# Optimization experiments

Measured on AMD Instinct MI355X. Metric: run time of the kernel, lower is better.

## Reference

```python
import jax, jax.numpy as jnp
import numpy as np

BASIS_PRIMES = (2, 3, 5, 7, 11, 13, 17, 19, 23, 29)


def _build_resonance(max_seq):
    # p-adic valuations v_p(n) for n = 1..max_seq, each basis prime (vectorized LUT build)
    n = np.arange(1, max_seq + 1, dtype=np.int64)
    vals = np.zeros((max_seq, len(BASIS_PRIMES)), dtype=np.float32)
    for j, p in enumerate(BASIS_PRIMES):
        m = n.copy()
        while True:
            div = (m % p) == 0
            if not div.any():
                break
            vals[div, j] += 1.0
            m = np.where(div, m // p, m)
    # resonance(a,b) = sum_i min(v_{p_i}(a), v_{p_i}(b))  -> [T, T]
    res = np.zeros((max_seq, max_seq), dtype=np.float32)
    for j in range(len(BASIS_PRIMES)):
        vj = vals[:, j]
        res += np.minimum(vj[:, None], vj[None, :])
    causal = np.tril(np.ones((max_seq, max_seq), dtype=bool))
    allowed = ((res > 0) | np.eye(max_seq, dtype=bool)) & causal
    bias = (np.log1p(res) * allowed).astype(np.float32)
    return bias, allowed


def setup_inputs() -> dict:
    B, T, d_model, head_size, max_seq = 8, 2048, 1024, 128, 2048
    key = jax.random.key(0)
    kx, kq, kk, kv = jax.random.split(key, 4)
    bound = 1.0 / np.sqrt(d_model)  # torch Linear default init range
    x = jax.random.normal(kx, (B, T, d_model), dtype=jnp.float32)
    Wq = jax.random.uniform(kq, (head_size, d_model), jnp.float32, -bound, bound)
    Wk = jax.random.uniform(kk, (head_size, d_model), jnp.float32, -bound, bound)
    Wv = jax.random.uniform(kv, (head_size, d_model), jnp.float32, -bound, bound)
    bias, allowed = _build_resonance(max_seq)
    return {
        "x": x, "Wq": Wq, "Wk": Wk, "Wv": Wv,
        "resonance_bias": jnp.asarray(bias),
        "allowed": jnp.asarray(allowed),
    }


def reference(x, Wq, Wk, Wv, resonance_bias, allowed):
    B, T, C = x.shape
    q = jnp.einsum('btc,hc->bth', x, Wq)
    k = jnp.einsum('btc,hc->bth', x, Wk)
    v = jnp.einsum('btc,hc->bth', x, Wv)
    # NOTE: original scales by C**-0.5 where C = d_model (input channels)
    wei = jnp.einsum('bth,bsh->bts', q, k) * (C ** -0.5)
    wei = wei + resonance_bias[:T, :T]
    neg = jnp.finfo(wei.dtype).min
    wei = jnp.where(allowed[:T, :T], wei, neg)
    wei = jax.nn.softmax(wei, axis=-1)  # dropout is identity in eval mode
    return jnp.einsum('bts,bsh->bth', wei, v)
```

## Files before the change

### kernel.cpp

```cpp
#include <hip/hip_runtime.h>
#include <hip/hip_bf16.h>
#include <stdint.h>

typedef float f32x4  __attribute__((ext_vector_type(4)));
typedef short s16x8  __attribute__((ext_vector_type(8)));
typedef short s16x4  __attribute__((ext_vector_type(4)));
typedef unsigned short u16x8 __attribute__((ext_vector_type(8)));

#define MFMA16(A,B,C) __builtin_amdgcn_mfma_f32_16x16x32_bf16((A),(B),(C),0,0,0)

__device__ __forceinline__ short f2bf(float f) {
    uint32_t u = __float_as_uint(f);
    u += 0x7FFFu + ((u >> 16) & 1u);
    return (short)(u >> 16);
}
__device__ __forceinline__ float bf2f(unsigned short u) {
    return __uint_as_float(((uint32_t)u) << 16);
}
__device__ __forceinline__ int cum_jobs(int qt) {
  int h = qt >> 1;
  return (qt & 1) ? (h + 1) * (h + 1) : h * (h + 1);
}

#define OFF_PB   0u
#define OFF_WPK  8388608u
#define OFF_PQ   9175040u
#define OFF_PK   13369344u
#define OFF_PV   17563648u
#define OFF_XPK  21757952u
#define OFF_PML  21757952u
#define OFF_PO   22863872u
#define WS_SPLIT 60096512u

__global__ __launch_bounds__(256) void pack_w_kernel(
    const float* __restrict__ wq, const float* __restrict__ wk,
    const float* __restrict__ wv, short* __restrict__ Wpk) {
  const int tid = threadIdx.x, wid = tid >> 6, lane = tid & 63;
  const int g = lane >> 4, c4 = lane & 15;
  const int idx = blockIdx.x * 4 + wid;
  const int im = idx >> 8, rest = idx & 255;
  const int ntl = rest >> 5, k32 = rest & 31;
  const float* w = (im == 0) ? wq : (im == 1) ? wk : wv;
  const float* p = w + (size_t)(ntl * 16 + c4) * 1024 + k32 * 32 + 4 * g;
  f32x4 lo = *(const f32x4*)p;
  f32x4 hi = *(const f32x4*)(p + 16);
  s16x8 o = { f2bf(lo[0]), f2bf(lo[1]), f2bf(lo[2]), f2bf(lo[3]),
              f2bf(hi[0]), f2bf(hi[1]), f2bf(hi[2]), f2bf(hi[3]) };
  *(s16x8*)(Wpk + (size_t)idx * 512 + lane * 8) = o;
}

__global__ __launch_bounds__(256) void pack_x_kernel(
    const float* __restrict__ x, short* __restrict__ xpk) {
  const int tid = threadIdx.x, wid = tid >> 6, lane = tid & 63;
  const int g = lane >> 4, c4 = lane & 15;
  const int idx = blockIdx.x * 4 + wid;
  const int m16 = idx >> 5, k32 = idx & 31;
  const float* p = x + (size_t)(m16 * 16 + c4) * 1024 + k32 * 32 + 4 * g;
  f32x4 lo = *(const f32x4*)p;
  f32x4 hi = *(const f32x4*)(p + 16);
  s16x8 o = { f2bf(lo[0]), f2bf(lo[1]), f2bf(lo[2]), f2bf(lo[3]),
              f2bf(hi[0]), f2bf(hi[1]), f2bf(hi[2]), f2bf(hi[3]) };
  *(s16x8*)(xpk + (size_t)idx * 512 + lane * 8) = o;
}

__global__ __launch_bounds__(256) void pack_bias_kernel(
    const float* __restrict__ bias, short* __restrict__ pb) {
  const int tid = threadIdx.x, wid = tid >> 6, lane = tid & 63;
  const int g = lane >> 4, c4 = lane & 15;
  const int idx = blockIdx.x * 4 + wid;
  const int t16 = idx >> 6, s32 = idx & 63;
  const int t = t16 * 16 + c4;
  const int sb = s32 * 32 + 4 * g;
  const float* p = bias + (size_t)t * 2048 + sb;
  f32x4 lo = *(const f32x4*)p;
  f32x4 hi = *(const f32x4*)(p + 16);
  s16x8 o;
  #pragma unroll
  for (int i = 0; i < 4; ++i) {
    int s0 = sb + i, s1 = sb + 16 + i;
    bool ok0 = (s0 <= t) && (s0 == t || lo[i] > 0.f);
    bool ok1 = (s1 <= t) && (s1 == t || hi[i] > 0.f);
    o[i]     = f2bf(ok0 ? lo[i] : -1e30f);
    o[4 + i] = f2bf(ok1 ? hi[i] : -1e30f);
  }
  *(s16x8*)(pb + (size_t)idx * 512 + lane * 8) = o;
}

__global__ __launch_bounds__(256, 3) void qkv_gemm6_kernel(
    const short* __restrict__ xpk, const short* __restrict__ Wpk,
    short* __restrict__ pq, short* __restrict__ pk, short* __restrict__ pv) {
  const int tid = threadIdx.x, wid = tid >> 6, lane = tid & 63;
  const int L8 = lane * 8;
  const int w = blockIdx.x * 4 + wid;
  const int im = w >> 9;
  const int t2 = w & 511;
  const int b = t2 >> 6;
  const short* xa = xpk + (size_t)(t2 * 64) * 512 + L8;
  const short* xb = xa + (size_t)32 * 512;
  const short* wp = Wpk + (size_t)(im * 256) * 512 + L8;

  f32x4 acc0[8], acc1[8];
  #pragma unroll
  for (int i = 0; i < 8; ++i) {
    acc0[i] = (f32x4){0.f, 0.f, 0.f, 0.f};
    acc1[i] = (f32x4){0.f, 0.f, 0.f, 0.f};
  }

  s16x8 xA0, xA1, wA[8], xB0, xB1, wB[8];
#define G6_LDX(d0, d1, kk) { d0 = *(const s16x8*)(xa + (size_t)(kk) * 512); \
                             d1 = *(const s16x8*)(xb + (size_t)(kk) * 512); }
#define G6_LDW(dw, kk) { _Pragma("unroll") \
    for (int nt = 0; nt < 8; ++nt) \
      dw[nt] = *(const s16x8*)(wp + (size_t)(nt * 32 + (kk)) * 512); }

  if (im < 2) {
    G6_LDX(xA0, xA1, 0); G6_LDW(wA, 0);
    for (int k = 0; k < 32; k += 2) {
      G6_LDX(xB0, xB1, k + 1); G6_LDW(wB, k + 1);
      #pragma unroll
      for (int nt = 0; nt < 8; ++nt) {
        acc0[nt] = MFMA16(wA[nt], xA0, acc0[nt]);
        acc1[nt] = MFMA16(wA[nt], xA1, acc1[nt]);
      }
      if (k + 2 < 32) { G6_LDX(xA0, xA1, k + 2); G6_LDW(wA, k + 2); }
      #pragma unroll
      for (int nt = 0; nt < 8; ++nt) {
        acc0[nt] = MFMA16(wB[nt], xB0, acc0[nt]);
        acc1[nt] = MFMA16(wB[nt], xB1, acc1[nt]);
      }
    }
    short* __restrict__ o = im ? pk : pq;
    const int loc0 = (t2 & 63) * 2;
    #pragma unroll
    for (int f = 0; f < 4; ++f) {
      s16x8 fr0 = { f2bf(acc0[2*f][0]),   f2bf(acc0[2*f][1]),
                    f2bf(acc0[2*f][2]),   f2bf(acc0[2*f][3]),
                    f2bf(acc0[2*f+1][0]), f2bf(acc0[2*f+1][1]),
                    f2bf(acc0[2*f+1][2]), f2bf(acc0[2*f+1][3]) };
      *(s16x8*)(o + (size_t)(b * 512 + loc0 * 4 + f) * 512 + L8) = fr0;
      s16x8 fr1 = { f2bf(acc1[2*f][0]),   f2bf(acc1[2*f][1]),
                    f2bf(acc1[2*f][2]),   f2bf(acc1[2*f][3]),
                    f2bf(acc1[2*f+1][0]), f2bf(acc1[2*f+1][1]),
                    f2bf(acc1[2*f+1][2]), f2bf(acc1[2*f+1][3]) };
      *(s16x8*)(o + (size_t)(b * 512 + (loc0 + 1) * 4 + f) * 512 + L8) = fr1;
    }
  } else {
    G6_LDX(xA0, xA1, 0); G6_LDW(wA, 0);
    for (int k = 0; k < 32; k += 2) {
      G6_LDX(xB0, xB1, k + 1); G6_LDW(wB, k + 1);
      #pragma unroll
      for (int nt = 0; nt < 8; ++nt) {
        acc0[nt] = MFMA16(xA0, wA[nt], acc0[nt]);
        acc1[nt] = MFMA16(xA1, wA[nt], acc1[nt]);
      }
      if (k + 2 < 32) { G6_LDX(xA0, xA1, k + 2); G6_LDW(wA, k + 2); }
      #pragma unroll
      for (int nt = 0; nt < 8; ++nt) {
        acc0[nt] = MFMA16(xB0, wB[nt], acc0[nt]);
        acc1[nt] = MFMA16(xB1, wB[nt], acc1[nt]);
      }
    }
    const int s32l = t2 & 63;
    #pragma unroll
    for (int nt = 0; nt < 8; ++nt) {
      s16x8 fr = { f2bf(acc0[nt][0]), f2bf(acc0[nt][1]),
                   f2bf(acc0[nt][2]), f2bf(acc0[nt][3]),
                   f2bf(acc1[nt][0]), f2bf(acc1[nt][1]),
                   f2bf(acc1[nt][2]), f2bf(acc1[nt][3]) };
      *(s16x8*)(pv + (size_t)(b * 512 + s32l * 8 + nt) * 512 + L8) = fr;
    }
  }
#undef G6_LDX
#undef G6_LDW
}

template<bool SPLIT>
__global__ __launch_bounds__(128) void attn_kernel(
    const short* __restrict__ pq, const short* __restrict__ pk,
    const short* __restrict__ pv, const short* __restrict__ pb,
    float* __restrict__ out, float* __restrict__ part_ml,
    short* __restrict__ part_o) {
  int qt, c;
  if (SPLIT) {
    const int i = blockIdx.x;
    int h = (int)sqrtf((float)i);
    while (h * h > i) --h;
    while ((h + 1) * (h + 1) <= i) ++h;
    if (i < h * (h + 1)) { qt = 2 * h - 1; c = i - h * h; }
    else                 { qt = 2 * h;     c = i - h * (h + 1); }
  } else {
    qt = blockIdx.x; c = 0;
  }
  const int n = (qt >> 1) + 1;
  const int tid = threadIdx.x;
  const int wid = tid >> 6, lane = tid & 63;
  const int g = lane >> 4, c4 = lane & 15;
  const int b = blockIdx.y;
  const int q16a = qt * 4 + wid * 2;
  const int L8 = lane * 8;

  s16x8 qfa[4], qfb[4];
  #pragma unroll
  for (int f = 0; f < 4; ++f) {
    qfa[f] = *(const s16x8*)(pq + (size_t)(b * 512 + q16a * 4 + f) * 512 + L8);
    qfb[f] = *(const s16x8*)(pq + (size_t)(b * 512 + (q16a + 1) * 4 + f) * 512 + L8);
  }

  float m0 = -1e30f, l0 = 0.f, m1 = -1e30f, l1 = 0.f;
  f32x4 acc0[8], acc1[8];
  #pragma unroll
  for (int i = 0; i < 8; ++i) {
    acc0[i] = (f32x4){0.f, 0.f, 0.f, 0.f};
    acc1[i] = (f32x4){0.f, 0.f, 0.f, 0.f};
  }

  const int q_hi_w = qt * 64 + wid * 32 + 32;
  const int s_begin = SPLIT ? c * 128 : 0;
  const int s_stop  = min(SPLIT ? s_begin + 128 : (1 << 30), q_hi_w);

  for (int s0 = s_begin; s0 < s_stop; s0 += 32) {
    const int s16i = s0 >> 4, s32 = s0 >> 5;
    const short* kbase = pk + (size_t)(b * 512 + s16i * 4) * 512 + L8;
    const short* vbase = pv + (size_t)(b * 512 + s32 * 8) * 512 + L8;
    s16x8 kf0[4], kf1[4];
    #pragma unroll
    for (int f = 0; f < 4; ++f) {
      kf0[f] = *(const s16x8*)(kbase + (size_t)f * 512);
      kf1[f] = *(const s16x8*)(kbase + (size_t)(4 + f) * 512);
    }
    u16x8 bva = *(const u16x8*)(pb + (size_t)(q16a * 64 + s32) * 512 + L8);
    u16x8 bvb = *(const u16x8*)(pb + (size_t)((q16a + 1) * 64 + s32) * 512 + L8);
    f32x4 s0a = (f32x4){0.f,0.f,0.f,0.f}, s1a = (f32x4){0.f,0.f,0.f,0.f};
    f32x4 s0b = (f32x4){0.f,0.f,0.f,0.f}, s1b = (f32x4){0.f,0.f,0.f,0.f};
    __builtin_amdgcn_s_setprio(1);
    #pragma unroll
    for (int f = 0; f < 4; ++f) {
      s0a = MFMA16(kf0[f], qfa[f], s0a);
      s1a = MFMA16(kf1[f], qfa[f], s1a);
      s0b = MFMA16(kf0[f], qfb[f], s0b);
      s1b = MFMA16(kf1[f], qfb[f], s1b);
    }
    __builtin_amdgcn_s_setprio(0);
    float va[8], vb[8];
    #pragma unroll
    for (int st = 0; st < 2; ++st)
      #pragma unroll
      for (int r = 0; r < 4; ++r) {
        va[st * 4 + r] = (st ? s1a[r] : s0a[r]) * 0.03125f + bf2f(bva[st * 4 + r]);
        vb[st * 4 + r] = (st ? s1b[r] : s0b[r]) * 0.03125f + bf2f(bvb[st * 4 + r]);
      }
    float mva = va[0], mvb = vb[0];
    #pragma unroll
    for (int i = 1; i < 8; ++i) { mva = fmaxf(mva, va[i]); mvb = fmaxf(mvb, vb[i]); }
    mva = fmaxf(mva, __shfl_xor(mva, 16)); mva = fmaxf(mva, __shfl_xor(mva, 32));
    mvb = fmaxf(mvb, __shfl_xor(mvb, 16)); mvb = fmaxf(mvb, __shfl_xor(mvb, 32));
    if (!__all((mva <= m0 + 8.f) && (mvb <= m1 + 8.f))) {
      float mn0 = fmaxf(m0, mva), mn1 = fmaxf(m1, mvb);
      float a0 = __expf(m0 - mn0), a1 = __expf(m1 - mn1);
      l0 *= a0; l1 *= a1; m0 = mn0; m1 = mn1;
      float ar0[4], ar1[4];
      #pragma unroll
      for (int r = 0; r < 4; ++r) {
        ar0[r] = __shfl(a0, (lane & 48) | (4 * g + r));
        ar1[r] = __shfl(a1, (lane & 48) | (4 * g + r));
      }
      #pragma unroll
      for (int nt = 0; nt < 8; ++nt)
        #pragma unroll
        for (int r = 0; r < 4; ++r) {
          acc0[nt][r] *= ar0[r];
          acc1[nt][r] *= ar1[r];
        }
    }
    float pa8[8], pb8[8], psa = 0.f, psb = 0.f;
    #pragma unroll
    for (int i = 0; i < 8; ++i) {
      pa8[i] = (va[i] > -1e29f) ? __expf(va[i] - m0) : 0.f;  psa += pa8[i];
      pb8[i] = (vb[i] > -1e29f) ? __expf(vb[i] - m1) : 0.f;  psb += pb8[i];
    }
    psa += __shfl_xor(psa, 16); psa += __shfl_xor(psa, 32); l0 += psa;
    psb += __shfl_xor(psb, 16); psb += __shfl_xor(psb, 32); l1 += psb;
    s16x8 paf = { f2bf(pa8[0]), f2bf(pa8[1]), f2bf(pa8[2]), f2bf(pa8[3]),
                  f2bf(pa8[4]), f2bf(pa8[5]), f2bf(pa8[6]), f2bf(pa8[7]) };
    s16x8 pbf = { f2bf(pb8[0]), f2bf(pb8[1]), f2bf(pb8[2]), f2bf(pb8[3]),
                  f2bf(pb8[4]), f2bf(pb8[5]), f2bf(pb8[6]), f2bf(pb8[7]) };
    __builtin_amdgcn_s_setprio(1);
    #pragma unroll
    for (int nt = 0; nt < 8; ++nt) {
      s16x8 vf = *(const s16x8*)(vbase + (size_t)nt * 512);
      acc0[nt] = MFMA16(paf, vf, acc0[nt]);
      acc1[nt] = MFMA16(pbf, vf, acc1[nt]);
    }
    __builtin_amdgcn_s_setprio(0);
  }

  if (!SPLIT || n == 1) {
    float li0 = 1.f / l0, li1 = 1.f / l1;
    float lr0[4], lr1[4];
    #pragma unroll
    for (int r = 0; r < 4; ++r) {
      lr0[r] = __shfl(li0, (lane & 48) | (4 * g + r));
      lr1[r] = __shfl(li1, (lane & 48) | (4 * g + r));
    }
    const int row0 = qt * 64 + wid * 32;
    #pragma unroll
    for (int nt = 0; nt < 8; ++nt)
      #pragma unroll
      for (int r = 0; r < 4; ++r) {
        out[(size_t)(b * 2048 + row0 + 4 * g + r) * 128 + 16 * nt + c4] =
            acc0[nt][r] * lr0[r];
        out[(size_t)(b * 2048 + row0 + 16 + 4 * g + r) * 128 + 16 * nt + c4] =
            acc1[nt][r] * lr1[r];
      }
  } else {
    const int slot = b * 270 + cum_jobs(qt) - 2 + c;
    short* po = part_o + (size_t)slot * 8192 + (size_t)(wid * 8) * 512 + L8;
    #pragma unroll
    for (int nt = 0; nt < 8; ++nt) {
      s16x8 fr = { f2bf(acc0[nt][0]), f2bf(acc0[nt][1]),
                   f2bf(acc0[nt][2]), f2bf(acc0[nt][3]),
                   f2bf(acc1[nt][0]), f2bf(acc1[nt][1]),
                   f2bf(acc1[nt][2]), f2bf(acc1[nt][3]) };
      *(s16x8*)(po + (size_t)nt * 512) = fr;
    }
    if (lane < 16) {
      part_ml[slot * 128 + wid * 32 + c4]           = m0;
      part_ml[slot * 128 + wid * 32 + 16 + c4]      = m1;
      part_ml[slot * 128 + 64 + wid * 32 + c4]      = l0;
      part_ml[slot * 128 + 64 + wid * 32 + 16 + c4] = l1;
    }
  }
}

__global__ __launch_bounds__(256) void combine_kernel(
    const float* __restrict__ part_ml, const unsigned short* __restrict__ part_o,
    float* __restrict__ out) {
  const int qt = 2 + blockIdx.x;
  const int b = blockIdx.y;
  const int n = (qt >> 1) + 1;
  const int slot0 = b * 270 + cum_jobs(qt) - 2;
  const int tid = threadIdx.x;

  __shared__ float scl[16][64];
  if (tid < 64) {
    const int r = tid;
    float M = -1e30f;
    for (int cc = 0; cc < n; ++cc)
      M = fmaxf(M, part_ml[(size_t)(slot0 + cc) * 128 + r]);
    float L = 0.f;
    for (int cc = 0; cc < n; ++cc)
      L += part_ml[(size_t)(slot0 + cc) * 128 + 64 + r] *
           __expf(part_ml[(size_t)(slot0 + cc) * 128 + r] - M);
    float inv = 1.f / L;
    for (int cc = 0; cc < n; ++cc)
      scl[cc][r] = __expf(part_ml[(size_t)(slot0 + cc) * 128 + r] - M) * inv;
  }
  __syncthreads();
  const int fgr = tid >> 6, lane = tid & 63;
  const int g = lane >> 4, c4 = lane & 15;
  for (int ff = fgr; ff < 16; ff += 4) {
    const int rbase = (ff >> 3) * 32 + 4 * g;
    const int col = (ff & 7) * 16 + c4;
    float o[8] = {0.f,0.f,0.f,0.f,0.f,0.f,0.f,0.f};
    for (int cc = 0; cc < n; ++cc) {
      u16x8 v = *(const u16x8*)(part_o +
          (size_t)(slot0 + cc) * 8192 + (size_t)ff * 512 + lane * 8);
      #pragma unroll
      for (int j = 0; j < 8; ++j)
        o[j] += bf2f(v[j]) * scl[cc][rbase + (j >> 2) * 16 + (j & 3)];
    }
    #pragma unroll
    for (int j = 0; j < 8; ++j) {
      const int row = rbase + (j >> 2) * 16 + (j & 3);
      out[(size_t)(b * 2048 + qt * 64 + row) * 128 + col] = o[j];
    }
  }
}

extern "C" void kernel_launch(void* const* d_in, const int* in_sizes, int n_in,
                              void* d_out, int out_size, void* d_ws, size_t ws_size,
                              hipStream_t stream) {
  const float* x    = (const float*)d_in[0];
  const float* wq   = (const float*)d_in[1];
  const float* wk   = (const float*)d_in[2];
  const float* wv   = (const float*)d_in[3];
  const float* bias = (const float*)d_in[4];

  char* ws = (char*)d_ws;
  short* pb      = (short*)(ws + OFF_PB);
  short* Wpk     = (short*)(ws + OFF_WPK);
  short* pq      = (short*)(ws + OFF_PQ);
  short* pk      = (short*)(ws + OFF_PK);
  short* pv      = (short*)(ws + OFF_PV);
  short* xpk     = (short*)(ws + OFF_XPK);
  float* part_ml = (float*)(ws + OFF_PML);
  short* part_o  = (short*)(ws + OFF_PO);
  float* outp    = (float*)d_out;

  pack_w_kernel<<<192, 256, 0, stream>>>(wq, wk, wv, Wpk);
  pack_x_kernel<<<8192, 256, 0, stream>>>(x, xpk);
  qkv_gemm6_kernel<<<384, 256, 0, stream>>>(xpk, Wpk, pq, pk, pv);
  pack_bias_kernel<<<2048, 256, 0, stream>>>(bias, pb);

  if (ws_size >= WS_SPLIT) {
    attn_kernel<true><<<dim3(272, 8), 128, 0, stream>>>(
        pq, pk, pv, pb, outp, part_ml, part_o);
    combine_kernel<<<dim3(30, 8), 256, 0, stream>>>(
        part_ml, (const unsigned short*)part_o, outp);
  } else {
    attn_kernel<false><<<dim3(32, 8), 128, 0, stream>>>(
        pq, pk, pv, pb, outp, part_ml, part_o);
  }
}
```

Measured before the change: 104.2 us.

## Fuse x bf16 conversion into QKV GEMM and merge weight/bias packing

The QKV GEMM now reads fp32 x directly and converts it to bf16 in registers, so the separate pack_x pass and its bf16 intermediate buffer go away. The weight and bias packing kernels are merged into a single launch, cutting launch count from four pre-attention kernels to two. In exchange, the GEMM loads twice the bytes for x, has to do the conversion inside its loop, and uses more registers (launch bounds occupancy hint lowered from 3 to 2). Each x row is read by three projection waves, so the raw fp32 x traffic is repeated.

Result: slower. 109.2 us (+4.8%).

```diff
diff --git a/kernel.cpp b/kernel.cpp
--- a/kernel.cpp
+++ b/kernel.cpp
@@ -27,76 +27,60 @@
 #define OFF_PQ   9175040u
 #define OFF_PK   13369344u
 #define OFF_PV   17563648u
-#define OFF_XPK  21757952u
 #define OFF_PML  21757952u
 #define OFF_PO   22863872u
 #define WS_SPLIT 60096512u
 
-__global__ __launch_bounds__(256) void pack_w_kernel(
+__global__ __launch_bounds__(256) void pack_misc_kernel(
     const float* __restrict__ wq, const float* __restrict__ wk,
-    const float* __restrict__ wv, short* __restrict__ Wpk) {
+    const float* __restrict__ wv, const float* __restrict__ bias,
+    short* __restrict__ Wpk, short* __restrict__ pb) {
   const int tid = threadIdx.x, wid = tid >> 6, lane = tid & 63;
   const int g = lane >> 4, c4 = lane & 15;
-  const int idx = blockIdx.x * 4 + wid;
-  const int im = idx >> 8, rest = idx & 255;
-  const int ntl = rest >> 5, k32 = rest & 31;
-  const float* w = (im == 0) ? wq : (im == 1) ? wk : wv;
-  const float* p = w + (size_t)(ntl * 16 + c4) * 1024 + k32 * 32 + 4 * g;
-  f32x4 lo = *(const f32x4*)p;
-  f32x4 hi = *(const f32x4*)(p + 16);
-  s16x8 o = { f2bf(lo[0]), f2bf(lo[1]), f2bf(lo[2]), f2bf(lo[3]),
-              f2bf(hi[0]), f2bf(hi[1]), f2bf(hi[2]), f2bf(hi[3]) };
-  *(s16x8*)(Wpk + (size_t)idx * 512 + lane * 8) = o;
-}
-
-__global__ __launch_bounds__(256) void pack_x_kernel(
-    const float* __restrict__ x, short* __restrict__ xpk) {
+  if (blockIdx.x < 192) {
+    const int idx = blockIdx.x * 4 + wid;
+    const int im = idx >> 8, rest = idx & 255;
+    const int ntl = rest >> 5, k32 = rest & 31;
+    const float* w = (im == 0) ? wq : (im == 1) ? wk : wv;
+    const float* p = w + (size_t)(ntl * 16 + c4) * 1024 + k32 * 32 + 4 * g;
+    f32x4 lo = *(const f32x4*)p;
+    f32x4 hi = *(const f32x4*)(p + 16);
+    s16x8 o = { f2bf(lo[0]), f2bf(lo[1]), f2bf(lo[2]), f2bf(lo[3]),
+                f2bf(hi[0]), f2bf(hi[1]), f2bf(hi[2]), f2bf(hi[3]) };
+    *(s16x8*)(Wpk + (size_t)idx * 512 + lane * 8) = o;
+  } else {
+    const int idx = (blockIdx.x - 192) * 4 + wid;
+    const int t16 = idx >> 6, s32 = idx & 63;
+    const int t = t16 * 16 + c4;
+    const int sb = s32 * 32 + 4 * g;
+    const float* p = bias + (size_t)t * 2048 + sb;
+    f32x4 lo = *(const f32x4*)p;
+    f32x4 hi = *(const f32x4*)(p + 16);
+    s16x8 o;
+    #pragma unroll
+    for (int i = 0; i < 4; ++i) {
+      int s0 = sb + i, s1 = sb + 16 + i;
+      bool ok0 = (s0 <= t) && (s0 == t || lo[i] > 0.f);
+      bool ok1 = (s1 <= t) && (s1 == t || hi[i] > 0.f);
+      o[i]     = f2bf(ok0 ? lo[i] : -1e30f);
+      o[4 + i] = f2bf(ok1 ? hi[i] : -1e30f);
+    }
+    *(s16x8*)(pb + (size_t)idx * 512 + lane * 8) = o;
+  }
+}
+
+__global__ __launch_bounds__(256, 2) void qkv_gemm7_kernel(
+    const float* __restrict__ x, const short* __restrict__ Wpk,
+    short* __restrict__ pq, short* __restrict__ pk, short* __restrict__ pv) {
   const int tid = threadIdx.x, wid = tid >> 6, lane = tid & 63;
   const int g = lane >> 4, c4 = lane & 15;
-  const int idx = blockIdx.x * 4 + wid;
-  const int m16 = idx >> 5, k32 = idx & 31;
-  const float* p = x + (size_t)(m16 * 16 + c4) * 1024 + k32 * 32 + 4 * g;
-  f32x4 lo = *(const f32x4*)p;
-  f32x4 hi = *(const f32x4*)(p + 16);
-  s16x8 o = { f2bf(lo[0]), f2bf(lo[1]), f2bf(lo[2]), f2bf(lo[3]),
-              f2bf(hi[0]), f2bf(hi[1]), f2bf(hi[2]), f2bf(hi[3]) };
-  *(s16x8*)(xpk + (size_t)idx * 512 + lane * 8) = o;
-}
-
-__global__ __launch_bounds__(256) void pack_bias_kernel(
-    const float* __restrict__ bias, short* __restrict__ pb) {
-  const int tid = threadIdx.x, wid = tid >> 6, lane = tid & 63;
-  const int g = lane >> 4, c4 = lane & 15;
-  const int idx = blockIdx.x * 4 + wid;
-  const int t16 = idx >> 6, s32 = idx & 63;
-  const int t = t16 * 16 + c4;
-  const int sb = s32 * 32 + 4 * g;
-  const float* p = bias + (size_t)t * 2048 + sb;
-  f32x4 lo = *(const f32x4*)p;
-  f32x4 hi = *(const f32x4*)(p + 16);
-  s16x8 o;
-  #pragma unroll
-  for (int i = 0; i < 4; ++i) {
-    int s0 = sb + i, s1 = sb + 16 + i;
-    bool ok0 = (s0 <= t) && (s0 == t || lo[i] > 0.f);
-    bool ok1 = (s1 <= t) && (s1 == t || hi[i] > 0.f);
-    o[i]     = f2bf(ok0 ? lo[i] : -1e30f);
-    o[4 + i] = f2bf(ok1 ? hi[i] : -1e30f);
-  }
-  *(s16x8*)(pb + (size_t)idx * 512 + lane * 8) = o;
-}
-
-__global__ __launch_bounds__(256, 3) void qkv_gemm6_kernel(
-    const short* __restrict__ xpk, const short* __restrict__ Wpk,
-    short* __restrict__ pq, short* __restrict__ pk, short* __restrict__ pv) {
-  const int tid = threadIdx.x, wid = tid >> 6, lane = tid & 63;
   const int L8 = lane * 8;
   const int w = blockIdx.x * 4 + wid;
   const int im = w >> 9;
   const int t2 = w & 511;
   const int b = t2 >> 6;
-  const short* xa = xpk + (size_t)(t2 * 64) * 512 + L8;
-  const short* xb = xa + (size_t)32 * 512;
+  const float* xrA = x + (size_t)(t2 * 32 + c4) * 1024 + 4 * g;
+  const float* xrB = xrA + (size_t)16 * 1024;
   const short* wp = Wpk + (size_t)(im * 256) * 512 + L8;
 
   f32x4 acc0[8], acc1[8];
@@ -106,27 +90,37 @@
     acc1[i] = (f32x4){0.f, 0.f, 0.f, 0.f};
   }
 
-  s16x8 xA0, xA1, wA[8], xB0, xB1, wB[8];
-#define G6_LDX(d0, d1, kk) { d0 = *(const s16x8*)(xa + (size_t)(kk) * 512); \
-                             d1 = *(const s16x8*)(xb + (size_t)(kk) * 512); }
-#define G6_LDW(dw, kk) { _Pragma("unroll") \
+  f32x4 aA0l, aA0h, aA1l, aA1h;
+  f32x4 aB0l, aB0h, aB1l, aB1h;
+  s16x8 wA[8], wB[8];
+#define G7_LDRAW(p0l, p0h, p1l, p1h, kk) { \
+    p0l = *(const f32x4*)(xrA + (size_t)(kk) * 32); \
+    p0h = *(const f32x4*)(xrA + (size_t)(kk) * 32 + 16); \
+    p1l = *(const f32x4*)(xrB + (size_t)(kk) * 32); \
+    p1h = *(const f32x4*)(xrB + (size_t)(kk) * 32 + 16); }
+#define G7_LDW(dw, kk) { _Pragma("unroll") \
     for (int nt = 0; nt < 8; ++nt) \
       dw[nt] = *(const s16x8*)(wp + (size_t)(nt * 32 + (kk)) * 512); }
+#define G7_CVT(fr, lo, hi) \
+    s16x8 fr = { f2bf(lo[0]), f2bf(lo[1]), f2bf(lo[2]), f2bf(lo[3]), \
+                 f2bf(hi[0]), f2bf(hi[1]), f2bf(hi[2]), f2bf(hi[3]) };
 
   if (im < 2) {
-    G6_LDX(xA0, xA1, 0); G6_LDW(wA, 0);
+    G7_LDRAW(aA0l, aA0h, aA1l, aA1h, 0); G7_LDW(wA, 0);
     for (int k = 0; k < 32; k += 2) {
-      G6_LDX(xB0, xB1, k + 1); G6_LDW(wB, k + 1);
+      G7_LDRAW(aB0l, aB0h, aB1l, aB1h, k + 1); G7_LDW(wB, k + 1);
+      G7_CVT(xf0, aA0l, aA0h); G7_CVT(xf1, aA1l, aA1h);
       #pragma unroll
       for (int nt = 0; nt < 8; ++nt) {
-        acc0[nt] = MFMA16(wA[nt], xA0, acc0[nt]);
-        acc1[nt] = MFMA16(wA[nt], xA1, acc1[nt]);
-      }
-      if (k + 2 < 32) { G6_LDX(xA0, xA1, k + 2); G6_LDW(wA, k + 2); }
+        acc0[nt] = MFMA16(wA[nt], xf0, acc0[nt]);
+        acc1[nt] = MFMA16(wA[nt], xf1, acc1[nt]);
+      }
+      if (k + 2 < 32) { G7_LDRAW(aA0l, aA0h, aA1l, aA1h, k + 2); G7_LDW(wA, k + 2); }
+      G7_CVT(yf0, aB0l, aB0h); G7_CVT(yf1, aB1l, aB1h);
       #pragma unroll
       for (int nt = 0; nt < 8; ++nt) {
-        acc0[nt] = MFMA16(wB[nt], xB0, acc0[nt]);
-        acc1[nt] = MFMA16(wB[nt], xB1, acc1[nt]);
+        acc0[nt] = MFMA16(wB[nt], yf0, acc0[nt]);
+        acc1[nt] = MFMA16(wB[nt], yf1, acc1[nt]);
       }
     }
     short* __restrict__ o = im ? pk : pq;
@@ -145,19 +139,21 @@
       *(s16x8*)(o + (size_t)(b * 512 + (loc0 + 1) * 4 + f) * 512 + L8) = fr1;
     }
   } else {
-    G6_LDX(xA0, xA1, 0); G6_LDW(wA, 0);
+    G7_LDRAW(aA0l, aA0h, aA1l, aA1h, 0); G7_LDW(wA, 0);
     for (int k = 0; k < 32; k += 2) {
-      G6_LDX(xB0, xB1, k + 1); G6_LDW(wB, k + 1);
+      G7_LDRAW(aB0l, aB0h, aB1l, aB1h, k + 1); G7_LDW(wB, k + 1);
+      G7_CVT(xf0, aA0l, aA0h); G7_CVT(xf1, aA1l, aA1h);
       #pragma unroll
       for (int nt = 0; nt < 8; ++nt) {
-        acc0[nt] = MFMA16(xA0, wA[nt], acc0[nt]);
-        acc1[nt] = MFMA16(xA1, wA[nt], acc1[nt]);
-      }
-      if (k + 2 < 32) { G6_LDX(xA0, xA1, k + 2); G6_LDW(wA, k + 2); }
+        acc0[nt] = MFMA16(xf0, wA[nt], acc0[nt]);
+        acc1[nt] = MFMA16(xf1, wA[nt], acc1[nt]);
+      }
+      if (k + 2 < 32) { G7_LDRAW(aA0l, aA0h, aA1l, aA1h, k + 2); G7_LDW(wA, k + 2); }
+      G7_CVT(yf0, aB0l, aB0h); G7_CVT(yf1, aB1l, aB1h);
       #pragma unroll
       for (int nt = 0; nt < 8; ++nt) {
-        acc0[nt] = MFMA16(xB0, wB[nt], acc0[nt]);
-        acc1[nt] = MFMA16(xB1, wB[nt], acc1[nt]);
+        acc0[nt] = MFMA16(yf0, wB[nt], acc0[nt]);
+        acc1[nt] = MFMA16(yf1, wB[nt], acc1[nt]);
       }
     }
     const int s32l = t2 & 63;
@@ -170,8 +166,9 @@
       *(s16x8*)(pv + (size_t)(b * 512 + s32l * 8 + nt) * 512 + L8) = fr;
     }
   }
-#undef G6_LDX
-#undef G6_LDW
+#undef G7_LDRAW
+#undef G7_LDW
+#undef G7_CVT
 }
 
 template<bool SPLIT>
@@ -392,15 +389,12 @@
   short* pq      = (short*)(ws + OFF_PQ);
   short* pk      = (short*)(ws + OFF_PK);
   short* pv      = (short*)(ws + OFF_PV);
-  short* xpk     = (short*)(ws + OFF_XPK);
   float* part_ml = (float*)(ws + OFF_PML);
   short* part_o  = (short*)(ws + OFF_PO);
   float* outp    = (float*)d_out;
 
-  pack_w_kernel<<<192, 256, 0, stream>>>(wq, wk, wv, Wpk);
-  pack_x_kernel<<<8192, 256, 0, stream>>>(x, xpk);
-  qkv_gemm6_kernel<<<384, 256, 0, stream>>>(xpk, Wpk, pq, pk, pv);
-  pack_bias_kernel<<<2048, 256, 0, stream>>>(bias, pb);
+  pack_misc_kernel<<<2240, 256, 0, stream>>>(wq, wk, wv, bias, Wpk, pb);
+  qkv_gemm7_kernel<<<384, 256, 0, stream>>>(x, Wpk, pq, pk, pv);
 
   if (ws_size >= WS_SPLIT) {
     attn_kernel<true><<<dim3(272, 8), 128, 0, stream>>>(
```
